# Kernel tuning notes

Hardware: AMD Instinct MI355X
Metric: run time of the kernel (lower is better)

Reference implementation:

```python
import jax, jax.numpy as jnp
import numpy as np

N = 50000   # nodes
E = 600000  # edges
D = 128     # input_nf == output_nf
H = 128     # hidden_nf


def _ln(x, g, b):
    m = x.mean(-1, keepdims=True)
    v = ((x - m) ** 2).mean(-1, keepdims=True)
    return (x - m) * jax.lax.rsqrt(v + 1e-5) * g + b


def setup_inputs() -> dict:
    key = jax.random.key(0)
    ks = jax.random.split(key, 10)

    def w(k, shape):
        return (jax.random.normal(k, shape, jnp.float32) / np.float32(np.sqrt(shape[0])))

    return dict(
        h=jax.random.normal(ks[0], (N, D), jnp.float32),
        edge_index=jax.random.randint(ks[1], (2, E), 0, N, dtype=jnp.int32),
        coord=jax.random.normal(ks[2], (N, 3), jnp.float32),
        node_ln_g=jnp.ones((D,), jnp.float32), node_ln_b=jnp.zeros((D,), jnp.float32),
        edge_ln_g=jnp.ones((H,), jnp.float32), edge_ln_b=jnp.zeros((H,), jnp.float32),
        edge_w1=w(ks[3], (2 * D + 1, H)), edge_b1=jnp.zeros((H,), jnp.float32),
        edge_w2=w(ks[4], (H, H)), edge_b2=jnp.zeros((H,), jnp.float32),
        node_w1=w(ks[5], (H + D, H)), node_b1=jnp.zeros((H,), jnp.float32),
        node_w2=w(ks[6], (H, D)), node_b2=jnp.zeros((D,), jnp.float32),
        coord_w1=w(ks[7], (H, H)), coord_b1=jnp.zeros((H,), jnp.float32),
        coord_w2=w(ks[8], (H, 1)) * 0.001,  # xavier gain=0.001, no bias
    )


def reference(h, edge_index, coord,
              node_ln_g, node_ln_b, edge_ln_g, edge_ln_b,
              edge_w1, edge_b1, edge_w2, edge_b2,
              node_w1, node_b1, node_w2, node_b2,
              coord_w1, coord_b1, coord_w2):
    row, col = edge_index[0], edge_index[1]
    n = h.shape[0]

    # coord2radial (normalize=False)
    coord_diff = coord[row] - coord[col]                    # [E,3]
    radial = jnp.sum(coord_diff ** 2, axis=1, keepdims=True)  # [E,1]

    h0 = h
    hn = _ln(h, node_ln_g, node_ln_b)                       # node LayerNorm

    # edge model: gather -> MLP (SiLU) -> LayerNorm
    e_in = jnp.concatenate([hn[row], hn[col], radial], axis=1)  # [E, 2D+1]
    e = jax.nn.silu(e_in @ edge_w1 + edge_b1)
    e = jax.nn.silu(e @ edge_w2 + edge_b2)
    e = _ln(e, edge_ln_g, edge_ln_b)                        # [E,H]

    # coord model: trans = coord_diff * coord_mlp(e); mean-aggregate by row
    scale = jax.nn.silu(e @ coord_w1 + coord_b1) @ coord_w2  # [E,1]
    trans = coord_diff * scale                               # [E,3]
    s = jax.ops.segment_sum(trans, row, num_segments=n)
    cnt = jax.ops.segment_sum(jnp.ones((trans.shape[0], 1), trans.dtype), row, num_segments=n)
    coord_out = coord + s / jnp.maximum(cnt, 1.0)

    # node model: scatter-add edge features, concat with h, MLP, residual
    agg = jax.ops.segment_sum(e, row, num_segments=n)        # [N,H]
    n_in = jnp.concatenate([hn, agg], axis=1)                # [N,H+D]
    h_out = jax.nn.silu(n_in @ node_w1 + node_b1) @ node_w2 + node_b2
    h_out = h0 + h_out                                       # residual
    return (h_out, coord_out)
```

## Files before the change

### kernel.cpp

```cpp
#include <hip/hip_runtime.h>
#include <math.h>

#define NN 50000
#define NE 600000

typedef __attribute__((ext_vector_type(8))) short bf16x8;
typedef __attribute__((ext_vector_type(4))) float f32x4;

__device__ __forceinline__ float silu_f(float x) {
    return x / (1.0f + __expf(-x));
}
__device__ __forceinline__ unsigned short f2bf(float x) {
    unsigned int u = __float_as_uint(x);
    return (unsigned short)((u + 0x7FFFu + ((u >> 16) & 1u)) >> 16);
}
__device__ __forceinline__ float bf2f(unsigned short s) {
    return __uint_as_float(((unsigned int)s) << 16);
}

__global__ __launch_bounds__(256) void hist_kernel(
    const int* __restrict__ erow, int* __restrict__ bins) {
    int i = blockIdx.x * 256 + threadIdx.x;
    if (i < NE) atomicAdd(&bins[erow[i]], 1);
}

__global__ __launch_bounds__(256) void scan1_kernel(
    const int* __restrict__ bins, int* __restrict__ bsum) {
    int gid = blockIdx.x * 256 + threadIdx.x;
    int v = (gid < NN) ? bins[gid] : 0;
    int lane = threadIdx.x & 63, wave = threadIdx.x >> 6;
#pragma unroll
    for (int d = 1; d < 64; d <<= 1) {
        int n = __shfl_up(v, d);
        if (lane >= d) v += n;
    }
    __shared__ int wsum[4];
    if (lane == 63) wsum[wave] = v;
    __syncthreads();
    if (threadIdx.x == 255) {
        bsum[blockIdx.x] = wsum[0] + wsum[1] + wsum[2] + wsum[3];
    }
}

__global__ void scan2_kernel(int* bsum, int nb) {
    if (threadIdx.x == 0 && blockIdx.x == 0) {
        int acc = 0;
        for (int i = 0; i < nb; i++) { int t = bsum[i]; bsum[i] = acc; acc += t; }
    }
}

__global__ __launch_bounds__(256) void scan3_kernel(
    const int* __restrict__ bins, const int* __restrict__ bsum,
    int* __restrict__ cur) {
    int gid = blockIdx.x * 256 + threadIdx.x;
    int v = (gid < NN) ? bins[gid] : 0;
    int lane = threadIdx.x & 63, wave = threadIdx.x >> 6;
    int inc = v;
#pragma unroll
    for (int d = 1; d < 64; d <<= 1) {
        int n = __shfl_up(inc, d);
        if (lane >= d) inc += n;
    }
    __shared__ int wsum[4];
    if (lane == 63) wsum[wave] = inc;
    __syncthreads();
    int wadd = 0;
    for (int w = 0; w < wave; w++) wadd += wsum[w];
    if (gid < NN) cur[gid] = bsum[blockIdx.x] + wadd + inc - v;
}

__global__ __launch_bounds__(256) void scatter_kernel(
    const int* __restrict__ erow, int* __restrict__ cur,
    int* __restrict__ perm) {
    int i = blockIdx.x * 256 + threadIdx.x;
    if (i < NE) {
        int r = erow[i];
        int pos = atomicAdd(&cur[r], 1);
        perm[pos] = i;
    }
}

__global__ __launch_bounds__(256) void prep_weights(
    const float* __restrict__ w1, const float* __restrict__ w2,
    const float* __restrict__ cw1, const float* __restrict__ nw1,
    const float* __restrict__ nw2,
    unsigned short* __restrict__ w1T, unsigned short* __restrict__ w2T,
    unsigned short* __restrict__ cw1T, unsigned short* __restrict__ nw1T,
    unsigned short* __restrict__ nw2T) {
    int i = blockIdx.x * 256 + threadIdx.x;
    if (i < 32768) { int n = i >> 8, k = i & 255; w1T[i] = f2bf(w1[k * 128 + n]); return; }
    int j = i - 32768;
    if (j < 16384) { int n = j >> 7, k = j & 127; w2T[j] = f2bf(w2[k * 128 + n]); return; }
    j -= 16384;
    if (j < 16384) { int n = j >> 7, k = j & 127; cw1T[j] = f2bf(cw1[k * 128 + n]); return; }
    j -= 16384;
    if (j < 32768) { int n = j >> 8, k = j & 255; nw1T[j] = f2bf(nw1[k * 128 + n]); return; }
    j -= 32768;
    if (j < 16384) { int n = j >> 7, k = j & 127; nw2T[j] = f2bf(nw2[k * 128 + n]); return; }
}

__global__ __launch_bounds__(256) void ln_nodes_kernel(
    const float* __restrict__ h, const float* __restrict__ g,
    const float* __restrict__ b, unsigned short* __restrict__ hnb) {
    int node = blockIdx.x * 4 + (threadIdx.x >> 6);
    int lane = threadIdx.x & 63;
    if (node >= NN) return;
    const float* row = h + (size_t)node * 128;
    float x0 = row[lane], x1 = row[lane + 64];
    float s = x0 + x1, s2 = x0 * x0 + x1 * x1;
#pragma unroll
    for (int off = 32; off; off >>= 1) {
        s  += __shfl_xor(s, off);
        s2 += __shfl_xor(s2, off);
    }
    float m = s * (1.0f / 128.0f);
    float v = s2 * (1.0f / 128.0f) - m * m;
    float inv = rsqrtf(v + 1e-5f);
    unsigned short* orow = hnb + (size_t)node * 128;
    orow[lane]      = f2bf((x0 - m) * inv * g[lane]      + b[lane]);
    orow[lane + 64] = f2bf((x1 - m) * inv * g[lane + 64] + b[lane + 64]);
}

__global__ __launch_bounds__(256, 2) void z_kernel(
    const unsigned short* __restrict__ hnb,
    const unsigned short* __restrict__ w1T,
    const float* __restrict__ b1,
    unsigned short* __restrict__ zrow, unsigned short* __restrict__ zcol) {
    __shared__ uint4 a1s[32 * 16];

    const int t    = threadIdx.x;
    const int lane = t & 63;
    const int wave = t >> 6;
    const int l15  = lane & 15;
    const int g4   = lane >> 4;
    const int n0   = wave * 32;
    const int sw   = l15 & 7;

    bf16x8 Btop[2][4], Bbot[2][4];
    float b1v[2];
#pragma unroll
    for (int nf = 0; nf < 2; nf++) {
        int wr = n0 + nf * 16 + l15;
        const unsigned short* p1 = w1T + wr * 256 + g4 * 8;
#pragma unroll
        for (int kc = 0; kc < 4; kc++) {
            Btop[nf][kc] = *(const bf16x8*)(p1 + kc * 32);
            Bbot[nf][kc] = *(const bf16x8*)(p1 + 128 + kc * 32);
        }
        b1v[nf] = b1[wr];
    }

    const int NT = (NN + 31) / 32;
    for (int tile = blockIdx.x; tile < NT; tile += gridDim.x) {
        const int n0t = tile * 32;
        int nn = NN - n0t; if (nn > 32) nn = 32;
        __syncthreads();
#pragma unroll
        for (int ii = 0; ii < 2; ii++) {
            int idx = t + ii * 256;
            int rr = idx >> 4, c = idx & 15;
            int node = n0t + ((rr < nn) ? rr : 0);
            a1s[rr * 16 + (c ^ (rr & 7))] =
                *(const uint4*)(hnb + (size_t)node * 128 + c * 8);
        }
        __syncthreads();

        f32x4 t00 = {0,0,0,0}, t01 = {0,0,0,0}, t10 = {0,0,0,0}, t11 = {0,0,0,0};
        f32x4 u00 = {0,0,0,0}, u01 = {0,0,0,0}, u10 = {0,0,0,0}, u11 = {0,0,0,0};
        {
            const bf16x8* A = (const bf16x8*)a1s;
#pragma unroll
            for (int kc = 0; kc < 4; kc++) {
                int ch = kc * 4 + g4;
                bf16x8 f0 = A[l15 * 16 + (ch ^ sw)];
                bf16x8 f1 = A[(l15 + 16) * 16 + (ch ^ sw)];
                t00 = __builtin_amdgcn_mfma_f32_16x16x32_bf16(f0, Btop[0][kc], t00, 0, 0, 0);
                t01 = __builtin_amdgcn_mfma_f32_16x16x32_bf16(f0, Btop[1][kc], t01, 0, 0, 0);
                t10 = __builtin_amdgcn_mfma_f32_16x16x32_bf16(f1, Btop[0][kc], t10, 0, 0, 0);
                t11 = __builtin_amdgcn_mfma_f32_16x16x32_bf16(f1, Btop[1][kc], t11, 0, 0, 0);
                u00 = __builtin_amdgcn_mfma_f32_16x16x32_bf16(f0, Bbot[0][kc], u00, 0, 0, 0);
                u01 = __builtin_amdgcn_mfma_f32_16x16x32_bf16(f0, Bbot[1][kc], u01, 0, 0, 0);
                u10 = __builtin_amdgcn_mfma_f32_16x16x32_bf16(f1, Bbot[0][kc], u10, 0, 0, 0);
                u11 = __builtin_amdgcn_mfma_f32_16x16x32_bf16(f1, Bbot[1][kc], u11, 0, 0, 0);
            }
        }
#pragma unroll
        for (int mf = 0; mf < 2; mf++) {
#pragma unroll
            for (int r = 0; r < 4; r++) {
                int row = mf * 16 + g4 * 4 + r;
                if (row < nn) {
                    int node = n0t + row;
#pragma unroll
                    for (int nf = 0; nf < 2; nf++) {
                        float tv = mf ? (nf ? t11[r] : t10[r]) : (nf ? t01[r] : t00[r]);
                        float uv = mf ? (nf ? u11[r] : u10[r]) : (nf ? u01[r] : u00[r]);
                        int col = n0 + nf * 16 + l15;
                        zrow[(size_t)node * 128 + col] = f2bf(tv + b1v[nf]);
                        zcol[(size_t)node * 128 + col] = f2bf(uv);
                    }
                }
            }
        }
    }
}

#define NWT (NE / 16)
#define WT_PER_XCD 4688
#define WPW 10
__global__ __launch_bounds__(256, 2) void edge_kernel(
    const unsigned short* __restrict__ zrow,
    const unsigned short* __restrict__ zcol,
    const int* __restrict__ erow, const int* __restrict__ ecol,
    const int* __restrict__ perm,
    const float* __restrict__ coord, const float* __restrict__ w1,
    const float* __restrict__ b2, const float* __restrict__ eg,
    const float* __restrict__ ebias, const float* __restrict__ cb1,
    const float* __restrict__ cw2,
    const unsigned short* __restrict__ w2T,
    const unsigned short* __restrict__ cw1T,
    float* __restrict__ agg, float* __restrict__ svec) {
    __shared__ uint4 wlds[4096];
    __shared__ uint4 ebuf4[4][256];

    const int t    = threadIdx.x;
    const int lane = t & 63;
    const int wave = t >> 6;
    const int l15  = lane & 15;
    const int g4   = lane >> 4;

#pragma unroll
    for (int i = 0; i < 16; i++) {
        int gi = t + i * 256;
        int m = gi >> 11, rem = gi & 2047;
        int col = rem >> 4, c = rem & 15;
        const unsigned short* src = (m ? cw1T : w2T) + col * 128 + c * 8;
        wlds[m * 2048 + col * 16 + (c ^ (col & 15))] = *(const uint4*)src;
    }

    float b2v[8], egv[8], ebv[8], cb1v[8], cw2v[8];
#pragma unroll
    for (int ng = 0; ng < 8; ng++) {
        int col = ng * 16 + l15;
        b2v[ng]  = b2[col];  egv[ng]  = eg[col]; ebv[ng] = ebias[col];
        cb1v[ng] = cb1[col]; cw2v[ng] = cw2[col];
    }
    bf16x8 w1r8[4];
#pragma unroll
    for (int kc = 0; kc < 4; kc++) {
        const float* p = w1 + 256 * 128 + kc * 32 + g4 * 8;
        bf16x8 v;
#pragma unroll
        for (int j = 0; j < 8; j++) v[j] = (short)f2bf(p[j]);
        w1r8[kc] = v;
    }
    __syncthreads();

    const bf16x8* WB  = (const bf16x8*)wlds;
    unsigned short* EBu = (unsigned short*)(&ebuf4[wave][0]);
    const bf16x8*  EBc = (const bf16x8*)EBu;

    const int xcd   = blockIdx.x & 7;
    const int wslot = (blockIdx.x >> 3) * 4 + wave;
    int base = xcd * WT_PER_XCD;
    int cap  = base + WT_PER_XCD; if (cap > NWT) cap = NWT;
    int wt0  = base + wslot * WPW;
    int wt1  = wt0 + WPW; if (wt1 > cap) wt1 = cap;

    for (int wt = wt0; wt < wt1; wt++) {
        const int e0 = wt * 16;
        int eid = perm[e0 + l15];
        int rid = erow[eid], cid = ecol[eid];
        float dx = coord[rid * 3 + 0] - coord[cid * 3 + 0];
        float dy = coord[rid * 3 + 1] - coord[cid * 3 + 1];
        float dz = coord[rid * 3 + 2] - coord[cid * 3 + 2];
        float rad = dx * dx + dy * dy + dz * dz;

        bf16x8 A2[4];
#pragma unroll
        for (int kc = 0; kc < 4; kc++) {
            bf16x8 zr = *(const bf16x8*)(zrow + (size_t)rid * 128 + kc * 32 + g4 * 8);
            bf16x8 zc = *(const bf16x8*)(zcol + (size_t)cid * 128 + kc * 32 + g4 * 8);
            bf16x8 o;
#pragma unroll
            for (int j = 0; j < 8; j++) {
                float x = bf2f((unsigned short)zr[j]) + bf2f((unsigned short)zc[j])
                        + rad * bf2f((unsigned short)w1r8[kc][j]);
                o[j] = (short)f2bf(silu_f(x));
            }
            A2[kc] = o;
        }
        f32x4 acc2[8];
#pragma unroll
        for (int ng = 0; ng < 8; ng++) {
            f32x4 a = {0, 0, 0, 0};
            int rowb = (ng * 16 + l15) * 16;
#pragma unroll
            for (int kc = 0; kc < 4; kc++)
                a = __builtin_amdgcn_mfma_f32_16x16x32_bf16(
                        A2[kc], WB[rowb + ((kc * 4 + g4) ^ l15)], a, 0, 0, 0);
            acc2[ng] = a;
        }
#pragma unroll
        for (int r = 0; r < 4; r++) {
            float sp = 0.0f, sq = 0.0f;
#pragma unroll
            for (int ng = 0; ng < 8; ng++) {
                float v = silu_f(acc2[ng][r] + b2v[ng]);
                acc2[ng][r] = v; sp += v; sq += v * v;
            }
            sp += __shfl_xor(sp, 1); sq += __shfl_xor(sq, 1);
            sp += __shfl_xor(sp, 2); sq += __shfl_xor(sq, 2);
            sp += __shfl_xor(sp, 4); sq += __shfl_xor(sq, 4);
            sp += __shfl_xor(sp, 8); sq += __shfl_xor(sq, 8);
            float m  = sp * (1.0f / 128.0f);
            float va = sq * (1.0f / 128.0f) - m * m;
            float inv = rsqrtf(va + 1e-5f);
#pragma unroll
            for (int ng = 0; ng < 8; ng++)
                acc2[ng][r] = (acc2[ng][r] - m) * inv * egv[ng] + ebv[ng];
        }
#pragma unroll
        for (int r = 0; r < 4; r++) {
            int er = g4 * 4 + r;
#pragma unroll
            for (int ng = 0; ng < 8; ng++) {
                int pos = ((ng * 2 + (l15 >> 3)) ^ er) & 15;
                EBu[er * 128 + pos * 8 + (l15 & 7)] = f2bf(acc2[ng][r]);
            }
        }
        {
            float accA[8];
#pragma unroll
            for (int ng = 0; ng < 8; ng++) accA[ng] = 0.0f;
            int curR = __shfl(rid, g4 * 4);
#pragma unroll
            for (int r = 0; r < 4; r++) {
                int rr = __shfl(rid, g4 * 4 + r);
                if (rr != curR) {
#pragma unroll
                    for (int ng = 0; ng < 8; ng++) {
                        atomicAdd(&agg[(size_t)curR * 128 + ng * 16 + l15], accA[ng]);
                        accA[ng] = 0.0f;
                    }
                    curR = rr;
                }
#pragma unroll
                for (int ng = 0; ng < 8; ng++) accA[ng] += acc2[ng][r];
            }
#pragma unroll
            for (int ng = 0; ng < 8; ng++)
                atomicAdd(&agg[(size_t)curR * 128 + ng * 16 + l15], accA[ng]);
        }
        bf16x8 A3[4];
#pragma unroll
        for (int kc = 0; kc < 4; kc++)
            A3[kc] = EBc[l15 * 16 + ((kc * 4 + g4) ^ l15)];
        f32x4 acc3[8];
#pragma unroll
        for (int ng = 0; ng < 8; ng++) {
            f32x4 a = {0, 0, 0, 0};
            int rowb = 2048 + (ng * 16 + l15) * 16;
#pragma unroll
            for (int kc = 0; kc < 4; kc++)
                a = __builtin_amdgcn_mfma_f32_16x16x32_bf16(
                        A3[kc], WB[rowb + ((kc * 4 + g4) ^ l15)], a, 0, 0, 0);
            acc3[ng] = a;
        }
#pragma unroll
        for (int r = 0; r < 4; r++) {
            float ps = 0.0f;
#pragma unroll
            for (int ng = 0; ng < 8; ng++)
                ps += silu_f(acc3[ng][r] + cb1v[ng]) * cw2v[ng];
            ps += __shfl_xor(ps, 1);
            ps += __shfl_xor(ps, 2);
            ps += __shfl_xor(ps, 4);
            ps += __shfl_xor(ps, 8);
            int er = g4 * 4 + r;
            int rr = __shfl(rid, er);
            float sx = __shfl(dx, er), sy = __shfl(dy, er), sz = __shfl(dz, er);
            if (l15 == 0)      atomicAdd(&svec[rr * 3 + 0], sx * ps);
            else if (l15 == 1) atomicAdd(&svec[rr * 3 + 1], sy * ps);
            else if (l15 == 2) atomicAdd(&svec[rr * 3 + 2], sz * ps);
        }
    }
}

__device__ __forceinline__ int swz128(int row, int col) {
    return row * 128 + (((col >> 3) ^ (row & 7)) << 3) + (col & 7);
}

__global__ __launch_bounds__(256, 2) void node_kernel(
    const float* __restrict__ h, const unsigned short* __restrict__ hnb,
    const float* __restrict__ aggp, const float* __restrict__ coord,
    const float* __restrict__ nb1, const float* __restrict__ nb2,
    const unsigned short* __restrict__ nw1T,
    const unsigned short* __restrict__ nw2T,
    const float* __restrict__ svec, const int* __restrict__ bins,
    float* __restrict__ hout, float* __restrict__ cout) {
    __shared__ uint4 a1s[32 * 32];
    __shared__ uint4 nbs[32 * 16];

    const int t    = threadIdx.x;
    const int lane = t & 63;
    const int wave = t >> 6;
    const int l15  = lane & 15;
    const int g4   = lane >> 4;
    const int n0   = wave * 32;
    const int sw   = l15 & 7;

    bf16x8 B1[2][8], B2[2][4];
    float nb1v[2], nb2v[2];
#pragma unroll
    for (int nf = 0; nf < 2; nf++) {
        int wr = n0 + nf * 16 + l15;
        const unsigned short* p1 = nw1T + wr * 256 + g4 * 8;
#pragma unroll
        for (int kc = 0; kc < 8; kc++) B1[nf][kc] = *(const bf16x8*)(p1 + kc * 32);
        const unsigned short* p2 = nw2T + wr * 128 + g4 * 8;
#pragma unroll
        for (int kc = 0; kc < 4; kc++) B2[nf][kc] = *(const bf16x8*)(p2 + kc * 32);
        nb1v[nf] = nb1[wr]; nb2v[nf] = nb2[wr];
    }
    unsigned short* nbu = (unsigned short*)nbs;

    const int NT = (NN + 31) / 32;
    for (int tile = blockIdx.x; tile < NT; tile += gridDim.x) {
        const int n0t = tile * 32;
        int nn = NN - n0t; if (nn > 32) nn = 32;

        if (t < 96) {
            int i = t / 3, j = t - (t / 3) * 3;
            int node = n0t + i;
            if (i < nn) {
                float c = fmaxf((float)bins[node], 1.0f);
                cout[node * 3 + j] = coord[node * 3 + j] + svec[node * 3 + j] / c;
            }
        }
        __syncthreads();
#pragma unroll
        for (int ii = 0; ii < 4; ii++) {
            int idx = t + ii * 256;
            int rr = idx >> 5, c = idx & 31;
            int node = n0t + ((rr < nn) ? rr : 0);
            uint4 d;
            if (c < 16) {
                d = *(const uint4*)(hnb + (size_t)node * 128 + c * 8);
            } else {
                const float* ap = aggp + (size_t)node * 128 + (c - 16) * 8;
                float4 f0 = *(const float4*)ap;
                float4 f1 = *(const float4*)(ap + 4);
                d.x = f2bf(f0.x) | ((unsigned)f2bf(f0.y) << 16);
                d.y = f2bf(f0.z) | ((unsigned)f2bf(f0.w) << 16);
                d.z = f2bf(f1.x) | ((unsigned)f2bf(f1.y) << 16);
                d.w = f2bf(f1.z) | ((unsigned)f2bf(f1.w) << 16);
            }
            a1s[rr * 32 + (c ^ (rr & 7))] = d;
        }
        __syncthreads();

        f32x4 a00 = {0,0,0,0}, a01 = {0,0,0,0}, a10 = {0,0,0,0}, a11 = {0,0,0,0};
        {
            const bf16x8* A = (const bf16x8*)a1s;
#pragma unroll
            for (int kc = 0; kc < 8; kc++) {
                int ch = kc * 4 + g4;
                bf16x8 f0 = A[l15 * 32 + (ch ^ sw)];
                bf16x8 f1 = A[(l15 + 16) * 32 + (ch ^ sw)];
                a00 = __builtin_amdgcn_mfma_f32_16x16x32_bf16(f0, B1[0][kc], a00, 0, 0, 0);
                a01 = __builtin_amdgcn_mfma_f32_16x16x32_bf16(f0, B1[1][kc], a01, 0, 0, 0);
                a10 = __builtin_amdgcn_mfma_f32_16x16x32_bf16(f1, B1[0][kc], a10, 0, 0, 0);
                a11 = __builtin_amdgcn_mfma_f32_16x16x32_bf16(f1, B1[1][kc], a11, 0, 0, 0);
            }
        }
#pragma unroll
        for (int mf = 0; mf < 2; mf++) {
#pragma unroll
            for (int r = 0; r < 4; r++) {
                int row = mf * 16 + g4 * 4 + r;
#pragma unroll
                for (int nf = 0; nf < 2; nf++) {
                    float v = mf ? (nf ? a11[r] : a10[r]) : (nf ? a01[r] : a00[r]);
                    v = silu_f(v + nb1v[nf]);
                    int col = n0 + nf * 16 + l15;
                    nbu[swz128(row, col)] = f2bf(v);
                }
            }
        }
        __syncthreads();

        f32x4 c00 = {0,0,0,0}, c01 = {0,0,0,0}, c10 = {0,0,0,0}, c11 = {0,0,0,0};
        {
            const bf16x8* A = (const bf16x8*)nbs;
#pragma unroll
            for (int kc = 0; kc < 4; kc++) {
                int ch = kc * 4 + g4;
                bf16x8 f0 = A[l15 * 16 + (ch ^ sw)];
                bf16x8 f1 = A[(l15 + 16) * 16 + (ch ^ sw)];
                c00 = __builtin_amdgcn_mfma_f32_16x16x32_bf16(f0, B2[0][kc], c00, 0, 0, 0);
                c01 = __builtin_amdgcn_mfma_f32_16x16x32_bf16(f0, B2[1][kc], c01, 0, 0, 0);
                c10 = __builtin_amdgcn_mfma_f32_16x16x32_bf16(f1, B2[0][kc], c10, 0, 0, 0);
                c11 = __builtin_amdgcn_mfma_f32_16x16x32_bf16(f1, B2[1][kc], c11, 0, 0, 0);
            }
        }
#pragma unroll
        for (int mf = 0; mf < 2; mf++) {
#pragma unroll
            for (int r = 0; r < 4; r++) {
                int row = mf * 16 + g4 * 4 + r;
                if (row < nn) {
                    int node = n0t + row;
#pragma unroll
                    for (int nf = 0; nf < 2; nf++) {
                        float v = mf ? (nf ? c11[r] : c10[r]) : (nf ? c01[r] : c00[r]);
                        int col = n0 + nf * 16 + l15;
                        hout[(size_t)node * 128 + col] =
                            v + nb2v[nf] + h[(size_t)node * 128 + col];
                    }
                }
            }
        }
    }
}

extern "C" void kernel_launch(void* const* d_in, const int* in_sizes, int n_in,
                              void* d_out, int out_size, void* d_ws, size_t ws_size,
                              hipStream_t stream) {
    const float* h     = (const float*)d_in[0];
    const int*   eidx  = (const int*)d_in[1];
    const float* coord = (const float*)d_in[2];
    const float* nlg   = (const float*)d_in[3];
    const float* nlb   = (const float*)d_in[4];
    const float* elg   = (const float*)d_in[5];
    const float* elb   = (const float*)d_in[6];
    const float* ew1   = (const float*)d_in[7];
    const float* eb1   = (const float*)d_in[8];
    const float* ew2   = (const float*)d_in[9];
    const float* eb2   = (const float*)d_in[10];
    const float* nw1   = (const float*)d_in[11];
    const float* nb1   = (const float*)d_in[12];
    const float* nw2   = (const float*)d_in[13];
    const float* nb2   = (const float*)d_in[14];
    const float* cw1   = (const float*)d_in[15];
    const float* cb1   = (const float*)d_in[16];
    const float* cw2   = (const float*)d_in[17];

    float* hout = (float*)d_out;
    float* cout = (float*)d_out + (size_t)NN * 128;

    char* ws = (char*)d_ws;
    unsigned short* hnb  = (unsigned short*)(ws);
    float*          agg  = (float*)(ws + 12800000);
    float*          svec = (float*)(ws + 38400000);
    int*            bins = (int*)(ws + 39000000);
    int*            cur  = (int*)(ws + 39200000);
    int*            bsum = (int*)(ws + 39400000);
    int*            perm = (int*)(ws + 39401024);
    unsigned short* w1T  = (unsigned short*)(ws + 41801024);
    unsigned short* w2T  = (unsigned short*)(ws + 41866560);
    unsigned short* cw1T = (unsigned short*)(ws + 41899328);
    unsigned short* nw1T = (unsigned short*)(ws + 41932096);
    unsigned short* nw2T = (unsigned short*)(ws + 41997632);
    unsigned short* zrow = (unsigned short*)(ws + 42030400);
    unsigned short* zcol = (unsigned short*)(ws + 54830400);

    hipMemsetAsync(agg, 0, (size_t)25600000 + 600000 + 200000, stream);

    const int* erow = eidx;
    const int* ecol = eidx + NE;

    const int NB = (NN + 255) / 256;

    hist_kernel<<<(NE + 255) / 256, 256, 0, stream>>>(erow, bins);
    scan1_kernel<<<NB, 256, 0, stream>>>(bins, bsum);
    scan2_kernel<<<1, 64, 0, stream>>>(bsum, NB);
    scan3_kernel<<<NB, 256, 0, stream>>>(bins, bsum, cur);
    scatter_kernel<<<(NE + 255) / 256, 256, 0, stream>>>(erow, cur, perm);

    prep_weights<<<448, 256, 0, stream>>>(ew1, ew2, cw1, nw1, nw2,
                                          w1T, w2T, cw1T, nw1T, nw2T);
    ln_nodes_kernel<<<(NN + 3) / 4, 256, 0, stream>>>(h, nlg, nlb, hnb);
    z_kernel<<<512, 256, 0, stream>>>(hnb, w1T, eb1, zrow, zcol);
    edge_kernel<<<1024, 256, 0, stream>>>(
        zrow, zcol, erow, ecol, perm, coord, ew1, eb2, elg, elb, cb1, cw2,
        w2T, cw1T, agg, svec);
    node_kernel<<<512, 256, 0, stream>>>(
        h, hnb, agg, coord, nb1, nb2, nw1T, nw2T, svec, bins, hout, cout);
}
```

Baseline: 531.4 us.

## Parallelize block-sum scan, enlarge edge blocks, interleave edge tiles, widen grids

The single-thread serial scan over block sums becomes a 256-thread wave-shuffle scan. The edge kernel now uses 1024-thread blocks with 16 waves sharing one copy of the LDS weights, which cuts the per-block weight staging. Each wave also takes strided edge tiles within its XCD's range instead of a contiguous chunk. The z and node kernels launch more blocks. The aim is to cut serial scan latency and redundant weight loads and to improve load balance, at the cost of possibly lower occupancy and register pressure at 1024 threads per block, and less row locality for agg atomics.

```diff
diff --git a/kernel.cpp b/kernel.cpp
--- a/kernel.cpp
+++ b/kernel.cpp
@@ -42,11 +42,22 @@
     }
 }
 
-__global__ void scan2_kernel(int* bsum, int nb) {
-    if (threadIdx.x == 0 && blockIdx.x == 0) {
-        int acc = 0;
-        for (int i = 0; i < nb; i++) { int t = bsum[i]; bsum[i] = acc; acc += t; }
-    }
+__global__ __launch_bounds__(256) void scan2_kernel(int* bsum, int nb) {
+    int t = threadIdx.x;
+    int lane = t & 63, wave = t >> 6;
+    int v = (t < nb) ? bsum[t] : 0;
+    int inc = v;
+#pragma unroll
+    for (int d = 1; d < 64; d <<= 1) {
+        int n = __shfl_up(inc, d);
+        if (lane >= d) inc += n;
+    }
+    __shared__ int ws[4];
+    if (lane == 63) ws[wave] = inc;
+    __syncthreads();
+    int add = 0;
+    for (int w = 0; w < wave; w++) add += ws[w];
+    if (t < nb) bsum[t] = add + inc - v;
 }
 
 __global__ __launch_bounds__(256) void scan3_kernel(
@@ -207,8 +218,9 @@
 
 #define NWT (NE / 16)
 #define WT_PER_XCD 4688
+#define WAVES_PER_XCD 512
 #define WPW 10
-__global__ __launch_bounds__(256, 2) void edge_kernel(
+__global__ __launch_bounds__(1024, 1) void edge_kernel(
     const unsigned short* __restrict__ zrow,
     const unsigned short* __restrict__ zcol,
     const int* __restrict__ erow, const int* __restrict__ ecol,
@@ -221,7 +233,7 @@
     const unsigned short* __restrict__ cw1T,
     float* __restrict__ agg, float* __restrict__ svec) {
     __shared__ uint4 wlds[4096];
-    __shared__ uint4 ebuf4[4][256];
+    __shared__ uint4 ebuf4[16][256];
 
     const int t    = threadIdx.x;
     const int lane = t & 63;
@@ -230,8 +242,8 @@
     const int g4   = lane >> 4;
 
 #pragma unroll
-    for (int i = 0; i < 16; i++) {
-        int gi = t + i * 256;
+    for (int i = 0; i < 4; i++) {
+        int gi = t + i * 1024;
         int m = gi >> 11, rem = gi & 2047;
         int col = rem >> 4, c = rem & 15;
         const unsigned short* src = (m ? cw1T : w2T) + col * 128 + c * 8;
@@ -260,14 +272,14 @@
     unsigned short* EBu = (unsigned short*)(&ebuf4[wave][0]);
     const bf16x8*  EBc = (const bf16x8*)EBu;
 
-    const int xcd   = blockIdx.x & 7;
-    const int wslot = (blockIdx.x >> 3) * 4 + wave;
-    int base = xcd * WT_PER_XCD;
-    int cap  = base + WT_PER_XCD; if (cap > NWT) cap = NWT;
-    int wt0  = base + wslot * WPW;
-    int wt1  = wt0 + WPW; if (wt1 > cap) wt1 = cap;
-
-    for (int wt = wt0; wt < wt1; wt++) {
+    const int xcd  = blockIdx.x & 7;
+    const int widx = (blockIdx.x >> 3) * 16 + wave;
+    const int base = xcd * WT_PER_XCD;
+    int cap = base + WT_PER_XCD; if (cap > NWT) cap = NWT;
+
+    for (int k = 0; k < WPW; k++) {
+        int wt = base + widx + k * WAVES_PER_XCD;
+        if (wt >= cap) break;
         const int e0 = wt * 16;
         int eid = perm[e0 + l15];
         int rid = erow[eid], cid = ecol[eid];
@@ -574,17 +586,17 @@
 
     hist_kernel<<<(NE + 255) / 256, 256, 0, stream>>>(erow, bins);
     scan1_kernel<<<NB, 256, 0, stream>>>(bins, bsum);
-    scan2_kernel<<<1, 64, 0, stream>>>(bsum, NB);
+    scan2_kernel<<<1, 256, 0, stream>>>(bsum, NB);
     scan3_kernel<<<NB, 256, 0, stream>>>(bins, bsum, cur);
     scatter_kernel<<<(NE + 255) / 256, 256, 0, stream>>>(erow, cur, perm);
 
     prep_weights<<<448, 256, 0, stream>>>(ew1, ew2, cw1, nw1, nw2,
                                           w1T, w2T, cw1T, nw1T, nw2T);
     ln_nodes_kernel<<<(NN + 3) / 4, 256, 0, stream>>>(h, nlg, nlb, hnb);
-    z_kernel<<<512, 256, 0, stream>>>(hnb, w1T, eb1, zrow, zcol);
-    edge_kernel<<<1024, 256, 0, stream>>>(
+    z_kernel<<<1563, 256, 0, stream>>>(hnb, w1T, eb1, zrow, zcol);
+    edge_kernel<<<256, 1024, 0, stream>>>(
         zrow, zcol, erow, ecol, perm, coord, ew1, eb2, elg, elb, cb1, cw2,
         w2T, cw1T, agg, svec);
-    node_kernel<<<512, 256, 0, stream>>>(
+    node_kernel<<<1563, 256, 0, stream>>>(
         h, hnb, agg, coord, nb1, nb2, nw1T, nw2T, svec, bins, hout, cout);
 }
```

Measured after the change: 607.1 us. 14.2% more time.
